# Kernel tuning notes

Measured on AMD Instinct MI355X. Metric: run time of the kernel, lower is better.

Reference implementation:

```python
import jax, jax.numpy as jnp
import numpy as np

B, W, H = 16384, 16, 16
NUM_CLASSES = 1024
EMBED = 4
OUT = 1024

def setup_inputs() -> dict:
    key = jax.random.key(0)
    k0, k1, k2 = jax.random.split(key, 3)
    x = jax.random.randint(k0, (B, W, H), 0, NUM_CLASSES, dtype=jnp.int32)
    W_embed = jax.random.normal(k1, (NUM_CLASSES, EMBED), dtype=jnp.float32) * 0.02
    b_embed = jnp.zeros((EMBED,), dtype=jnp.float32)
    W_dense = jax.random.normal(k2, (EMBED * W * H, OUT), dtype=jnp.float32) * 0.02
    b_dense = jnp.zeros((OUT,), dtype=jnp.float32)
    return {"x": x, "W_embed": W_embed, "b_embed": b_embed, "W_dense": W_dense, "b_dense": b_dense}

def reference(x, W_embed, b_embed, W_dense, b_dense):
    # one_hot(x, C) @ W_embed + b_embed is mathematically a row-gather of W_embed
    emb = W_embed[x] + b_embed                 # (B, W, H, EMBED)
    flat = emb.reshape(emb.shape[0], -1)        # (B, W*H*EMBED)  == rearrange '... w h c -> ... (w h c)'
    return flat @ W_dense + b_dense             # (B, OUT)
```

## Files before the change

kernel.cpp:

```cpp
#include <hip/hip_runtime.h>
#include <stdint.h>
#include <stddef.h>

typedef __attribute__((ext_vector_type(8))) short bf16x8;
typedef __attribute__((ext_vector_type(8))) unsigned short u16x8;
typedef __attribute__((ext_vector_type(4))) float f32x4;

typedef const __attribute__((address_space(1))) void* gptr1_t;
typedef __attribute__((address_space(3))) void* lptr3_t;

#define GLOAD_LDS16(gp, lp) \
  __builtin_amdgcn_global_load_lds((gptr1_t)(gp), (lptr3_t)(lp), 16, 0, 0)

__device__ __forceinline__ uint16_t f2bf(float f) {
  uint32_t u = __builtin_bit_cast(uint32_t, f);
  u += 0x7fffu + ((u >> 16) & 1u);
  return (uint16_t)(u >> 16);
}

#define MB   16384
#define NP   256
#define KDIM 1024
#define NDIM 1024

__global__ void build_a_kernel(const int* __restrict__ x,
                               const float* __restrict__ We,
                               const float* __restrict__ be,
                               uint16_t* __restrict__ A) {
  const int t = blockIdx.x * 256 + threadIdx.x;
  const int2 cls = ((const int2*)x)[t];
  const float4 e0 = *(const float4*)(We + (size_t)cls.x * 4);
  const float4 e1 = *(const float4*)(We + (size_t)cls.y * 4);
  const float4 bb = *(const float4*)be;
  u16x8 o = { f2bf(e0.x + bb.x), f2bf(e0.y + bb.y), f2bf(e0.z + bb.z), f2bf(e0.w + bb.w),
              f2bf(e1.x + bb.x), f2bf(e1.y + bb.y), f2bf(e1.z + bb.z), f2bf(e1.w + bb.w) };
  *(u16x8*)(A + (size_t)t * 8) = o;
}

__global__ void build_bt_kernel(const float* __restrict__ Wd,
                                uint16_t* __restrict__ Bt) {
  __shared__ uint16_t tile[32][33];
  const int k0 = blockIdx.y * 32;
  const int n0 = blockIdx.x * 32;
  const int tx = threadIdx.x;
  const int ty = threadIdx.y;
  #pragma unroll
  for (int r = 0; r < 32; r += 8)
    tile[ty + r][tx] = f2bf(Wd[(size_t)(k0 + ty + r) * NDIM + n0 + tx]);
  __syncthreads();
  #pragma unroll
  for (int r = 0; r < 32; r += 8)
    Bt[(size_t)(n0 + ty + r) * KDIM + k0 + tx] = tile[tx][ty + r];
}

#define BM  128
#define BN  128
#define BKH 32
#define BK  64
#define NK  (KDIM / BK)

__global__ __launch_bounds__(256) void gemm_bt_kernel(
    const uint16_t* __restrict__ A,
    const uint16_t* __restrict__ Bt,
    const float* __restrict__ bias,
    float* __restrict__ C) {
  __shared__ uint16_t As[2][BM * BKH];
  __shared__ uint16_t Bs[2][BN * BKH];

  const int tid  = threadIdx.x;
  const int bm   = blockIdx.x;
  const int bn   = blockIdx.y;
  const int wave = tid >> 6;
  const int lane = tid & 63;
  const int wr   = wave >> 1;
  const int wc   = wave & 1;
  const int lm   = lane & 15;
  const int q    = lane >> 4;

  const int row0 = bm * BM;
  const int col0 = bn * BN;

  const int srow = tid >> 2;
  const int scol = (tid & 3) * 8;

  f32x4 acc[4][4];
  #pragma unroll
  for (int i = 0; i < 4; i++)
    #pragma unroll
    for (int j = 0; j < 4; j++)
      acc[i][j] = (f32x4){0.f, 0.f, 0.f, 0.f};

  for (int kt = 0; kt < NK; ++kt) {
    const int k0 = kt * BK;
    #pragma unroll
    for (int h = 0; h < 2; ++h) {
      GLOAD_LDS16(A  + (size_t)(row0      + srow) * KDIM + k0 + h * BKH + scol, As[h] + tid * 8);
      GLOAD_LDS16(A  + (size_t)(row0 + 64 + srow) * KDIM + k0 + h * BKH + scol, As[h] + 2048 + tid * 8);
      GLOAD_LDS16(Bt + (size_t)(col0      + srow) * KDIM + k0 + h * BKH + scol, Bs[h] + tid * 8);
      GLOAD_LDS16(Bt + (size_t)(col0 + 64 + srow) * KDIM + k0 + h * BKH + scol, Bs[h] + 2048 + tid * 8);
    }
    __syncthreads();

    #pragma unroll
    for (int h = 0; h < 2; ++h) {
      bf16x8 af[4], bfr[4];
      #pragma unroll
      for (int i = 0; i < 4; i++)
        af[i] = *(const bf16x8*)(As[h] + (wr * 64 + i * 16 + lm) * BKH + q * 8);
      #pragma unroll
      for (int j = 0; j < 4; j++)
        bfr[j] = *(const bf16x8*)(Bs[h] + (wc * 64 + j * 16 + lm) * BKH + q * 8);

      #pragma unroll
      for (int i = 0; i < 4; i++)
        #pragma unroll
        for (int j = 0; j < 4; j++)
          acc[i][j] = __builtin_amdgcn_mfma_f32_16x16x32_bf16(af[i], bfr[j], acc[i][j], 0, 0, 0);
    }

    __syncthreads();
  }

  float bvals[4];
  #pragma unroll
  for (int j = 0; j < 4; j++)
    bvals[j] = bias[col0 + wc * 64 + j * 16 + lm];

  #pragma unroll
  for (int i = 0; i < 4; i++) {
    const int rbase = row0 + wr * 64 + i * 16 + q * 4;
    #pragma unroll
    for (int j = 0; j < 4; j++) {
      const int col = col0 + wc * 64 + j * 16 + lm;
      #pragma unroll
      for (int r = 0; r < 4; r++)
        C[(size_t)(rbase + r) * NDIM + col] = acc[i][j][r] + bvals[j];
    }
  }
}

__global__ void naive_kernel(const int* __restrict__ x,
                             const float* __restrict__ We,
                             const float* __restrict__ be,
                             const float* __restrict__ Wd,
                             const float* __restrict__ bd,
                             float* __restrict__ out) {
  __shared__ float emb[KDIM];
  const int b = blockIdx.x;
  const int tid = threadIdx.x;
  {
    const int cls = x[(size_t)b * NP + tid];
    const float4 e  = *(const float4*)(We + (size_t)cls * 4);
    const float4 bb = *(const float4*)be;
    emb[tid * 4 + 0] = e.x + bb.x;
    emb[tid * 4 + 1] = e.y + bb.y;
    emb[tid * 4 + 2] = e.z + bb.z;
    emb[tid * 4 + 3] = e.w + bb.w;
  }
  __syncthreads();
  float acc0 = bd[tid], acc1 = bd[tid + 256], acc2 = bd[tid + 512], acc3 = bd[tid + 768];
  for (int k = 0; k < KDIM; ++k) {
    const float a = emb[k];
    const float* w = Wd + (size_t)k * NDIM + tid;
    acc0 += a * w[0];
    acc1 += a * w[256];
    acc2 += a * w[512];
    acc3 += a * w[768];
  }
  float* o = out + (size_t)b * NDIM + tid;
  o[0] = acc0; o[256] = acc1; o[512] = acc2; o[768] = acc3;
}

extern "C" void kernel_launch(void* const* d_in, const int* in_sizes, int n_in,
                              void* d_out, int out_size, void* d_ws, size_t ws_size,
                              hipStream_t stream) {
  const int*   x  = (const int*)d_in[0];
  const float* We = (const float*)d_in[1];
  const float* be = (const float*)d_in[2];
  const float* Wd = (const float*)d_in[3];
  const float* bd = (const float*)d_in[4];
  float* out = (float*)d_out;

  const size_t needA = (size_t)MB * KDIM * sizeof(uint16_t);
  const size_t needB = (size_t)NDIM * KDIM * sizeof(uint16_t);

  if (ws_size >= needA + needB) {
    uint16_t* Aw  = (uint16_t*)d_ws;
    uint16_t* Btw = (uint16_t*)((char*)d_ws + needA);
    build_a_kernel<<<MB * NP / 2 / 256, 256, 0, stream>>>(x, We, be, Aw);
    build_bt_kernel<<<dim3(NDIM / 32, KDIM / 32), dim3(32, 8), 0, stream>>>(Wd, Btw);
    gemm_bt_kernel<<<dim3(MB / BM, NDIM / BN), 256, 0, stream>>>(Aw, Btw, bd, out);
  } else {
    naive_kernel<<<MB, 256, 0, stream>>>(x, We, be, Wd, bd, out);
  }
}
```

Baseline: 136.3 us.

## Fuse embedding gather into GEMM via LDS-resident bf16 embedding table

Drops the separate kernel that built a bf16 activation matrix in workspace. Each GEMM block now converts the small embedding table (plus bias) to bf16 in LDS, streams the integer class indices through LDS, and gathers the A fragments directly from that table. The index loads for the next k-tile are prefetched into registers. This avoids writing and re-reading a large intermediate activation matrix. In exchange every column block re-reads the indices, rebuilds the table, and performs scattered LDS gathers that may cause bank conflicts.

```diff
diff --git a/kernel.cpp b/kernel.cpp
--- a/kernel.cpp
+++ b/kernel.cpp
@@ -3,7 +3,7 @@
 #include <stddef.h>
 
 typedef __attribute__((ext_vector_type(8))) short bf16x8;
-typedef __attribute__((ext_vector_type(8))) unsigned short u16x8;
+typedef __attribute__((ext_vector_type(4))) short bf16x4;
 typedef __attribute__((ext_vector_type(4))) float f32x4;
 
 typedef const __attribute__((address_space(1))) void* gptr1_t;
@@ -22,20 +22,13 @@
 #define NP   256
 #define KDIM 1024
 #define NDIM 1024
-
-__global__ void build_a_kernel(const int* __restrict__ x,
-                               const float* __restrict__ We,
-                               const float* __restrict__ be,
-                               uint16_t* __restrict__ A) {
-  const int t = blockIdx.x * 256 + threadIdx.x;
-  const int2 cls = ((const int2*)x)[t];
-  const float4 e0 = *(const float4*)(We + (size_t)cls.x * 4);
-  const float4 e1 = *(const float4*)(We + (size_t)cls.y * 4);
-  const float4 bb = *(const float4*)be;
-  u16x8 o = { f2bf(e0.x + bb.x), f2bf(e0.y + bb.y), f2bf(e0.z + bb.z), f2bf(e0.w + bb.w),
-              f2bf(e1.x + bb.x), f2bf(e1.y + bb.y), f2bf(e1.z + bb.z), f2bf(e1.w + bb.w) };
-  *(u16x8*)(A + (size_t)t * 8) = o;
-}
+#define NCLS 1024
+
+#define BM  128
+#define BN  128
+#define BKH 32
+#define BK  64
+#define NK  (KDIM / BK)
 
 __global__ void build_bt_kernel(const float* __restrict__ Wd,
                                 uint16_t* __restrict__ Bt) {
@@ -53,18 +46,15 @@
     Bt[(size_t)(n0 + ty + r) * KDIM + k0 + tx] = tile[tx][ty + r];
 }
 
-#define BM  128
-#define BN  128
-#define BKH 32
-#define BK  64
-#define NK  (KDIM / BK)
-
-__global__ __launch_bounds__(256) void gemm_bt_kernel(
-    const uint16_t* __restrict__ A,
+__global__ __launch_bounds__(256) void fused_gemm_kernel(
+    const int* __restrict__ x,
+    const float* __restrict__ We,
+    const float* __restrict__ be,
     const uint16_t* __restrict__ Bt,
     const float* __restrict__ bias,
     float* __restrict__ C) {
-  __shared__ uint16_t As[2][BM * BKH];
+  __shared__ uint16_t web[NCLS * 4];
+  __shared__ int      xs[8 * 256];
   __shared__ uint16_t Bs[2][BN * BKH];
 
   const int tid  = threadIdx.x;
@@ -80,8 +70,24 @@
   const int row0 = bm * BM;
   const int col0 = bn * BN;
 
-  const int srow = tid >> 2;
-  const int scol = (tid & 3) * 8;
+  {
+    const float4 bb = *(const float4*)be;
+    for (int c = tid; c < NCLS; c += 256) {
+      const float4 w = *(const float4*)(We + (size_t)c * 4);
+      bf16x4 t;
+      t[0] = (short)f2bf(w.x + bb.x);
+      t[1] = (short)f2bf(w.y + bb.y);
+      t[2] = (short)f2bf(w.z + bb.z);
+      t[3] = (short)f2bf(w.w + bb.w);
+      *(bf16x4*)(web + (size_t)c * 4) = t;
+    }
+  }
+
+  const int srow  = tid >> 2;
+  const int scol  = (tid & 3) * 8;
+  const int xrow  = tid >> 2;
+  const int xpos4 = (tid & 3) * 4;
+  const int p2w   = (tid & 3) * 2;
 
   f32x4 acc[4][4];
   #pragma unroll
@@ -90,23 +96,50 @@
     for (int j = 0; j < 4; j++)
       acc[i][j] = (f32x4){0.f, 0.f, 0.f, 0.f};
 
+  const int* xrp_a = x + (size_t)(row0      + xrow) * NP;
+  const int* xrp_b = x + (size_t)(row0 + 64 + xrow) * NP;
+
+  int4 xqa = *(const int4*)(xrp_a + xpos4);
+  int4 xqb = *(const int4*)(xrp_b + xpos4);
+
+  const int xrd_base = (q << 8) + ((wr * 64 + lm) << 1);
+
   for (int kt = 0; kt < NK; ++kt) {
+    {
+      const int ra2 = xrow * 2;
+      const int rb2 = (64 + xrow) * 2;
+      int2 v;
+      v.x = xqa.x; v.y = xqa.y; *(int2*)(xs + (p2w    ) * 256 + ra2) = v;
+      v.x = xqa.z; v.y = xqa.w; *(int2*)(xs + (p2w + 1) * 256 + ra2) = v;
+      v.x = xqb.x; v.y = xqb.y; *(int2*)(xs + (p2w    ) * 256 + rb2) = v;
+      v.x = xqb.z; v.y = xqb.w; *(int2*)(xs + (p2w + 1) * 256 + rb2) = v;
+    }
+
     const int k0 = kt * BK;
     #pragma unroll
     for (int h = 0; h < 2; ++h) {
-      GLOAD_LDS16(A  + (size_t)(row0      + srow) * KDIM + k0 + h * BKH + scol, As[h] + tid * 8);
-      GLOAD_LDS16(A  + (size_t)(row0 + 64 + srow) * KDIM + k0 + h * BKH + scol, As[h] + 2048 + tid * 8);
       GLOAD_LDS16(Bt + (size_t)(col0      + srow) * KDIM + k0 + h * BKH + scol, Bs[h] + tid * 8);
       GLOAD_LDS16(Bt + (size_t)(col0 + 64 + srow) * KDIM + k0 + h * BKH + scol, Bs[h] + 2048 + tid * 8);
     }
+
+    if (kt + 1 < NK) {
+      xqa = *(const int4*)(xrp_a + (kt + 1) * 16 + xpos4);
+      xqb = *(const int4*)(xrp_b + (kt + 1) * 16 + xpos4);
+    }
+
     __syncthreads();
 
     #pragma unroll
     for (int h = 0; h < 2; ++h) {
       bf16x8 af[4], bfr[4];
       #pragma unroll
-      for (int i = 0; i < 4; i++)
-        af[i] = *(const bf16x8*)(As[h] + (wr * 64 + i * 16 + lm) * BKH + q * 8);
+      for (int i = 0; i < 4; i++) {
+        const int2 xp = *(const int2*)(xs + xrd_base + (h << 10) + (i << 5));
+        union { bf16x8 v; struct { bf16x4 lo, hi; } s; } u;
+        u.s.lo = *(const bf16x4*)(web + (((unsigned)xp.x) << 2));
+        u.s.hi = *(const bf16x4*)(web + (((unsigned)xp.y) << 2));
+        af[i] = u.v;
+      }
       #pragma unroll
       for (int j = 0; j < 4; j++)
         bfr[j] = *(const bf16x8*)(Bs[h] + (wc * 64 + j * 16 + lm) * BKH + q * 8);
@@ -181,15 +214,12 @@
   const float* bd = (const float*)d_in[4];
   float* out = (float*)d_out;
 
-  const size_t needA = (size_t)MB * KDIM * sizeof(uint16_t);
   const size_t needB = (size_t)NDIM * KDIM * sizeof(uint16_t);
 
-  if (ws_size >= needA + needB) {
-    uint16_t* Aw  = (uint16_t*)d_ws;
-    uint16_t* Btw = (uint16_t*)((char*)d_ws + needA);
-    build_a_kernel<<<MB * NP / 2 / 256, 256, 0, stream>>>(x, We, be, Aw);
+  if (ws_size >= needB) {
+    uint16_t* Btw = (uint16_t*)d_ws;
     build_bt_kernel<<<dim3(NDIM / 32, KDIM / 32), dim3(32, 8), 0, stream>>>(Wd, Btw);
-    gemm_bt_kernel<<<dim3(MB / BM, NDIM / BN), 256, 0, stream>>>(Aw, Btw, bd, out);
+    fused_gemm_kernel<<<dim3(MB / BM, NDIM / BN), 256, 0, stream>>>(x, We, be, Btw, bd, out);
   } else {
     naive_kernel<<<MB, 256, 0, stream>>>(x, We, be, Wd, bd, out);
   }
```

Measured after the change: 131.9 us. -3.3%, faster.
